# Performance work log

Hardware: AMD Instinct MI355X
Metric: run time of the kernel (lower is better)

Reference implementation:

```python
import jax, jax.numpy as jnp
import numpy as np

VOCAB, EMBED, HIDDEN, LAYERS = 256, 32, 32, 10
B, T = 1024, 1024


def setup_inputs() -> dict:
    key = jax.random.key(0)
    ks = jax.random.split(key, 8)
    s_e = 1.0  # nn.Embedding default init is N(0,1); scale others like uniform fan-in
    k_rnn = 1.0 / np.sqrt(HIDDEN)
    k_fc = 1.0 / np.sqrt(HIDDEN)
    x = jax.random.randint(ks[0], (B, T), 0, VOCAB, dtype=jnp.int64) if jax.config.jax_enable_x64 else jax.random.randint(ks[0], (B, T), 0, VOCAB, dtype=jnp.int32)
    emb = jax.random.normal(ks[1], (VOCAB, EMBED), dtype=jnp.float32) * s_e
    W_ih = jax.random.uniform(ks[2], (LAYERS, HIDDEN, EMBED), jnp.float32, -k_rnn, k_rnn)
    W_hh = jax.random.uniform(ks[3], (LAYERS, HIDDEN, HIDDEN), jnp.float32, -k_rnn, k_rnn)
    b_ih = jax.random.uniform(ks[4], (LAYERS, HIDDEN), jnp.float32, -k_rnn, k_rnn)
    b_hh = jax.random.uniform(ks[5], (LAYERS, HIDDEN), jnp.float32, -k_rnn, k_rnn)
    W_fc = jax.random.uniform(ks[6], (VOCAB, HIDDEN), jnp.float32, -k_fc, k_fc)
    b_fc = jax.random.uniform(ks[7], (VOCAB,), jnp.float32, -k_fc, k_fc)
    return {"x": x, "emb": emb, "W_ih": W_ih, "W_hh": W_hh,
            "b_ih": b_ih, "b_hh": b_hh, "W_fc": W_fc, "b_fc": b_fc}


def reference(x, emb, W_ih, W_hh, b_ih, b_hh, W_fc, b_fc):
    # Embedding lookup: [B, T, E]
    xe = emb[x]
    L = W_ih.shape[0]
    Bn = x.shape[0]
    h0 = jnp.zeros((L, Bn, W_hh.shape[-1]), dtype=xe.dtype)

    def step(h, xt):
        # h: [L, B, H]; xt: [B, E]
        inp = xt
        new_h = []
        for l in range(L):  # sequential across layers (true dependency)
            hl = jnp.tanh(inp @ W_ih[l].T + b_ih[l] + h[l] @ W_hh[l].T + b_hh[l])
            new_h.append(hl)
            inp = hl
        return jnp.stack(new_h), None

    hT, _ = jax.lax.scan(step, h0, jnp.swapaxes(xe, 0, 1))  # scan over T
    # out[:, -1, :] of top RNN layer == final hidden of last layer
    return hT[-1] @ W_fc.T + b_fc
```

## Files before the change

kernel.cpp:

```cpp
#include <hip/hip_runtime.h>

#define VOCABSZ 256
#define EMBED   32
#define HIDDEN  32
#define LAYERS  10
#define BATCH   1024
#define SEQ     1024
#define BPB     16
#define U       4
#define NITER   (SEQ / U + LAYERS - 1)

typedef _Float16 f16x8 __attribute__((ext_vector_type(8)));
typedef float    f32x4 __attribute__((ext_vector_type(4)));
typedef _Float16 h2    __attribute__((ext_vector_type(2)));

__device__ __forceinline__ unsigned pk(float a, float b) {
    h2 t; t[0] = (_Float16)a; t[1] = (_Float16)b;
    return __builtin_bit_cast(unsigned, t);
}
__device__ __forceinline__ f16x8 u2f(uint4 u) { return __builtin_bit_cast(f16x8, u); }

__device__ __forceinline__ float th(float c, float b2) {
    const float t = __builtin_fmaf(c, 2.8853900817779268f, b2);
#if __has_builtin(__builtin_amdgcn_exp2f)
    const float e = __builtin_amdgcn_exp2f(t);
#else
    const float e = __expf(0.6931471805599453f * t);
#endif
    const float r = __builtin_amdgcn_rcpf(1.0f + e);
    return __builtin_fmaf(-2.0f, r, 1.0f);
}

__device__ __forceinline__ uint4 mk_nat(const float* row, int g) {
    const float4 a = *(const float4*)(row + 8 * g);
    const float4 b = *(const float4*)(row + 8 * g + 4);
    return uint4{pk(a.x, a.y), pk(a.z, a.w), pk(b.x, b.y), pk(b.z, b.w)};
}
__device__ __forceinline__ uint4 mk_kp(const float* row, int g) {
    const float4 a = *(const float4*)(row + 4 * g);
    const float4 b = *(const float4*)(row + 16 + 4 * g);
    return uint4{pk(a.x, a.y), pk(a.z, a.w), pk(b.x, b.y), pk(b.z, b.w)};
}

__global__ __launch_bounds__(640, 1) void rnn_mfma(
    const int* __restrict__ x, const float* __restrict__ emb,
    const float* __restrict__ W_ih, const float* __restrict__ W_hh,
    const float* __restrict__ b_ih, const float* __restrict__ b_hh,
    float* __restrict__ h_out)
{
    __shared__ __align__(16) unsigned char hb[2 * LAYERS * U * 1024];

    const int tid   = threadIdx.x;
    const int w     = tid >> 6;
    const int lane  = tid & 63;
    const int bc    = lane & 15;
    const int g     = lane >> 4;
    const int bbase = blockIdx.x * BPB;

    for (int i = tid; i < (int)sizeof(hb) / 4; i += 640)
        ((unsigned*)hb)[i] = 0u;

    const float* ri0 = W_ih + (w * HIDDEN + bc)      * EMBED;
    const float* ri1 = W_ih + (w * HIDDEN + 16 + bc) * EMBED;
    const float* rh0 = W_hh + (w * HIDDEN + bc)      * HIDDEN;
    const float* rh1 = W_hh + (w * HIDDEN + 16 + bc) * HIDDEN;
    const uint4 wf00 = (w == 0) ? mk_nat(ri0, g) : mk_kp(ri0, g);
    const uint4 wf10 = (w == 0) ? mk_nat(ri1, g) : mk_kp(ri1, g);
    const uint4 wf01 = mk_kp(rh0, g);
    const uint4 wf11 = mk_kp(rh1, g);

    float bias2[8];
    #pragma unroll
    for (int m = 0; m < 2; ++m)
        #pragma unroll
        for (int r = 0; r < 4; ++r) {
            const int hid = w * HIDDEN + m * 16 + g * 4 + r;
            bias2[m * 4 + r] = 2.8853900817779268f * (b_ih[hid] + b_hh[hid]);
        }

    #define SL(p, l, u) ((((p) * LAYERS + (l)) * U + (u)) * 1024)
    const int off = g * 256 + bc * 16;

    uint4  cur[U];
    float4 eraw[U][2];
    int4   tok_pf;
    if (w == 0) {
        const int4 t4 = *(const int4*)(x + (bbase + bc) * SEQ);
        const int tk[U] = {t4.x, t4.y, t4.z, t4.w};
        #pragma unroll
        for (int u = 0; u < U; ++u) {
            const float4* ep = (const float4*)(emb + tk[u] * EMBED + g * 8);
            const float4 e0 = ep[0], e1 = ep[1];
            cur[u] = uint4{pk(e0.x, e0.y), pk(e0.z, e0.w), pk(e1.x, e1.y), pk(e1.z, e1.w)};
        }
        tok_pf = *(const int4*)(x + (bbase + bc) * SEQ + U);
    }

    uint4 bown = uint4{0, 0, 0, 0};

    auto body = [&](int it, int P) {
        __syncthreads();
        const int tb = (it - w) * U;
        if (tb < 0 || tb >= SEQ) return;

        const bool pf = (w == 0) && (tb + U < SEQ);
        if (pf) {
            const int tk[U] = {tok_pf.x, tok_pf.y, tok_pf.z, tok_pf.w};
            #pragma unroll
            for (int u = 0; u < U; ++u) {
                const float4* ep = (const float4*)(emb + tk[u] * EMBED + g * 8);
                eraw[u][0] = ep[0]; eraw[u][1] = ep[1];
            }
            if (tb + 2 * U < SEQ)
                tok_pf = *(const int4*)(x + (bbase + bc) * SEQ + tb + 2 * U);
        }

        uint4 bin[U];
        if (w == 0) {
            #pragma unroll
            for (int u = 0; u < U; ++u) bin[u] = cur[u];
        } else {
            #pragma unroll
            for (int u = 0; u < U; ++u)
                bin[u] = *(const uint4*)(hb + SL(P ^ 1, w - 1, u) + off);
        }
        f32x4 cin0[U], cin1[U];
        const f32x4 z = {0.f, 0.f, 0.f, 0.f};
        #pragma unroll
        for (int u = 0; u < U; ++u) {
            cin0[u] = __builtin_amdgcn_mfma_f32_16x16x32_f16(u2f(wf00), u2f(bin[u]), z, 0, 0, 0);
            cin1[u] = __builtin_amdgcn_mfma_f32_16x16x32_f16(u2f(wf10), u2f(bin[u]), z, 0, 0, 0);
        }

        #pragma unroll
        for (int u = 0; u < U; ++u) {
            const f32x4 c0 = __builtin_amdgcn_mfma_f32_16x16x32_f16(u2f(wf01), u2f(bown), cin0[u], 0, 0, 0);
            const f32x4 c1 = __builtin_amdgcn_mfma_f32_16x16x32_f16(u2f(wf11), u2f(bown), cin1[u], 0, 0, 0);

            float hv[8];
            #pragma unroll
            for (int r = 0; r < 4; ++r) {
                hv[r]     = th(c0[r], bias2[r]);
                hv[4 + r] = th(c1[r], bias2[4 + r]);
            }
            bown = uint4{pk(hv[0], hv[1]), pk(hv[2], hv[3]),
                         pk(hv[4], hv[5]), pk(hv[6], hv[7])};

            if (w < LAYERS - 1)
                *(uint4*)(hb + SL(P, w, u) + off) = bown;

            if (w == LAYERS - 1 && tb + u == SEQ - 1) {
                #pragma unroll
                for (int r = 0; r < 4; ++r) {
                    h_out[(bbase + bc) * HIDDEN + g * 4 + r]      = hv[r];
                    h_out[(bbase + bc) * HIDDEN + 16 + g * 4 + r] = hv[4 + r];
                }
            }
        }

        if (pf) {
            #pragma unroll
            for (int u = 0; u < U; ++u) {
                const float4 e0 = eraw[u][0], e1 = eraw[u][1];
                cur[u] = uint4{pk(e0.x, e0.y), pk(e0.z, e0.w), pk(e1.x, e1.y), pk(e1.z, e1.w)};
            }
        }
    };

    for (int it = 0; it < NITER + 1; it += 2) {
        body(it, 0);
        body(it + 1, 1);
    }
    #undef SL
}

__global__ __launch_bounds__(256) void rnn_fc(
    const float* __restrict__ h_fin, const float* __restrict__ W_fc,
    const float* __restrict__ b_fc, float* __restrict__ out)
{
    const int b = blockIdx.x;
    const int v = threadIdx.x;
    const float4* hr = (const float4*)(h_fin + b * HIDDEN);
    const float4* wr = (const float4*)(W_fc + v * HIDDEN);
    float acc = b_fc[v];
    #pragma unroll
    for (int c = 0; c < 8; ++c) {
        const float4 hv = hr[c], wv = wr[c];
        acc += hv.x * wv.x + hv.y * wv.y + hv.z * wv.z + hv.w * wv.w;
    }
    out[b * VOCABSZ + v] = acc;
}

extern "C" void kernel_launch(void* const* d_in, const int* in_sizes, int n_in,
                              void* d_out, int out_size, void* d_ws, size_t ws_size,
                              hipStream_t stream) {
    const int*   x    = (const int*)d_in[0];
    const float* emb  = (const float*)d_in[1];
    const float* W_ih = (const float*)d_in[2];
    const float* W_hh = (const float*)d_in[3];
    const float* b_ih = (const float*)d_in[4];
    const float* b_hh = (const float*)d_in[5];
    const float* W_fc = (const float*)d_in[6];
    const float* b_fc = (const float*)d_in[7];
    float* out   = (float*)d_out;
    float* h_fin = (float*)d_ws;

    rnn_mfma<<<BATCH / BPB, 640, 0, stream>>>(x, emb, W_ih, W_hh, b_ih, b_hh, h_fin);
    rnn_fc<<<BATCH, VOCABSZ, 0, stream>>>(h_fin, W_fc, b_fc, out);
}
```

Baseline: 535.0 us.

## Fuse final FC projection into RNN kernel via MFMA and double per-step unroll

Removes the separate FC kernel: the last layer's final hidden state is staged in shared memory and each wavefront computes 16-vocab tiles of the output projection with MFMA, then adds the bias. The timestep unroll U goes from 4 to 8, which halves the number of wavefront-pipeline stages and __syncthreads barriers but doubles the per-stage register and LDS buffers. The shared buffer drops the unused last-layer slot to offset part of that LDS growth. Risks are more register pressure and a longer pipeline fill and drain per stage.

```diff
diff --git a/kernel.cpp b/kernel.cpp
--- a/kernel.cpp
+++ b/kernel.cpp
@@ -7,8 +7,8 @@
 #define BATCH   1024
 #define SEQ     1024
 #define BPB     16
-#define U       4
-#define NITER   (SEQ / U + LAYERS - 1)
+#define U       8
+#define NBODY   (SEQ / U + LAYERS)
 
 typedef _Float16 f16x8 __attribute__((ext_vector_type(8)));
 typedef float    f32x4 __attribute__((ext_vector_type(4)));
@@ -42,13 +42,15 @@
     return uint4{pk(a.x, a.y), pk(a.z, a.w), pk(b.x, b.y), pk(b.z, b.w)};
 }
 
-__global__ __launch_bounds__(640, 1) void rnn_mfma(
+__global__ __launch_bounds__(640, 1) void rnn_fused(
     const int* __restrict__ x, const float* __restrict__ emb,
     const float* __restrict__ W_ih, const float* __restrict__ W_hh,
     const float* __restrict__ b_ih, const float* __restrict__ b_hh,
-    float* __restrict__ h_out)
+    const float* __restrict__ W_fc, const float* __restrict__ b_fc,
+    float* __restrict__ out)
 {
-    __shared__ __align__(16) unsigned char hb[2 * LAYERS * U * 1024];
+    __shared__ __align__(16) unsigned char hb[2 * (LAYERS - 1) * U * 1024];
+    __shared__ __align__(16) unsigned char fcs[1024];
 
     const int tid   = threadIdx.x;
     const int w     = tid >> 6;
@@ -78,25 +80,29 @@
             bias2[m * 4 + r] = 2.8853900817779268f * (b_ih[hid] + b_hh[hid]);
         }
 
-    #define SL(p, l, u) ((((p) * LAYERS + (l)) * U + (u)) * 1024)
+    #define SL(p, l, u_) ((((p) * (LAYERS - 1) + (l)) * U + (u_)) * 1024)
     const int off = g * 256 + bc * 16;
 
     uint4  cur[U];
     float4 eraw[U][2];
-    int4   tok_pf;
+    int    tokpf[U];
+    const int* xp = x + (bbase + bc) * SEQ;
     if (w == 0) {
-        const int4 t4 = *(const int4*)(x + (bbase + bc) * SEQ);
-        const int tk[U] = {t4.x, t4.y, t4.z, t4.w};
+        const int4 a = *(const int4*)(xp), b = *(const int4*)(xp + 4);
+        const int tk[U] = {a.x, a.y, a.z, a.w, b.x, b.y, b.z, b.w};
         #pragma unroll
         for (int u = 0; u < U; ++u) {
             const float4* ep = (const float4*)(emb + tk[u] * EMBED + g * 8);
             const float4 e0 = ep[0], e1 = ep[1];
             cur[u] = uint4{pk(e0.x, e0.y), pk(e0.z, e0.w), pk(e1.x, e1.y), pk(e1.z, e1.w)};
         }
-        tok_pf = *(const int4*)(x + (bbase + bc) * SEQ + U);
+        const int4 c = *(const int4*)(xp + 8), d = *(const int4*)(xp + 12);
+        tokpf[0] = c.x; tokpf[1] = c.y; tokpf[2] = c.z; tokpf[3] = c.w;
+        tokpf[4] = d.x; tokpf[5] = d.y; tokpf[6] = d.z; tokpf[7] = d.w;
     }
 
     uint4 bown = uint4{0, 0, 0, 0};
+    const f32x4 z = {0.f, 0.f, 0.f, 0.f};
 
     auto body = [&](int it, int P) {
         __syncthreads();
@@ -105,14 +111,17 @@
 
         const bool pf = (w == 0) && (tb + U < SEQ);
         if (pf) {
-            const int tk[U] = {tok_pf.x, tok_pf.y, tok_pf.z, tok_pf.w};
             #pragma unroll
             for (int u = 0; u < U; ++u) {
-                const float4* ep = (const float4*)(emb + tk[u] * EMBED + g * 8);
+                const float4* ep = (const float4*)(emb + tokpf[u] * EMBED + g * 8);
                 eraw[u][0] = ep[0]; eraw[u][1] = ep[1];
             }
-            if (tb + 2 * U < SEQ)
-                tok_pf = *(const int4*)(x + (bbase + bc) * SEQ + tb + 2 * U);
+            if (tb + 2 * U < SEQ) {
+                const int4 c = *(const int4*)(xp + tb + 2 * U);
+                const int4 d = *(const int4*)(xp + tb + 2 * U + 4);
+                tokpf[0] = c.x; tokpf[1] = c.y; tokpf[2] = c.z; tokpf[3] = c.w;
+                tokpf[4] = d.x; tokpf[5] = d.y; tokpf[6] = d.z; tokpf[7] = d.w;
+            }
         }
 
         uint4 bin[U];
@@ -125,7 +134,6 @@
                 bin[u] = *(const uint4*)(hb + SL(P ^ 1, w - 1, u) + off);
         }
         f32x4 cin0[U], cin1[U];
-        const f32x4 z = {0.f, 0.f, 0.f, 0.f};
         #pragma unroll
         for (int u = 0; u < U; ++u) {
             cin0[u] = __builtin_amdgcn_mfma_f32_16x16x32_f16(u2f(wf00), u2f(bin[u]), z, 0, 0, 0);
@@ -148,14 +156,6 @@
 
             if (w < LAYERS - 1)
                 *(uint4*)(hb + SL(P, w, u) + off) = bown;
-
-            if (w == LAYERS - 1 && tb + u == SEQ - 1) {
-                #pragma unroll
-                for (int r = 0; r < 4; ++r) {
-                    h_out[(bbase + bc) * HIDDEN + g * 4 + r]      = hv[r];
-                    h_out[(bbase + bc) * HIDDEN + 16 + g * 4 + r] = hv[4 + r];
-                }
-            }
         }
 
         if (pf) {
@@ -167,28 +167,26 @@
         }
     };
 
-    for (int it = 0; it < NITER + 1; it += 2) {
+    for (int it = 0; it < NBODY; it += 2) {
         body(it, 0);
         body(it + 1, 1);
     }
     #undef SL
-}
-
-__global__ __launch_bounds__(256) void rnn_fc(
-    const float* __restrict__ h_fin, const float* __restrict__ W_fc,
-    const float* __restrict__ b_fc, float* __restrict__ out)
-{
-    const int b = blockIdx.x;
-    const int v = threadIdx.x;
-    const float4* hr = (const float4*)(h_fin + b * HIDDEN);
-    const float4* wr = (const float4*)(W_fc + v * HIDDEN);
-    float acc = b_fc[v];
+
+    if (w == LAYERS - 1) *(uint4*)(fcs + off) = bown;
+    __syncthreads();
+    const uint4 bfc = *(const uint4*)(fcs + off);
     #pragma unroll
-    for (int c = 0; c < 8; ++c) {
-        const float4 hv = hr[c], wv = wr[c];
-        acc += hv.x * wv.x + hv.y * wv.y + hv.z * wv.z + hv.w * wv.w;
+    for (int rep = 0; rep < 2; ++rep) {
+        const int vt = w + rep * LAYERS;
+        if (vt < VOCABSZ / 16) {
+            const uint4 afc = mk_kp(W_fc + (vt * 16 + bc) * HIDDEN, g);
+            const f32x4 c = __builtin_amdgcn_mfma_f32_16x16x32_f16(u2f(afc), u2f(bfc), z, 0, 0, 0);
+            const float4 b4 = *(const float4*)(b_fc + vt * 16 + 4 * g);
+            const float4 o  = {c[0] + b4.x, c[1] + b4.y, c[2] + b4.z, c[3] + b4.w};
+            *(float4*)(out + (bbase + bc) * VOCABSZ + vt * 16 + 4 * g) = o;
+        }
     }
-    out[b * VOCABSZ + v] = acc;
 }
 
 extern "C" void kernel_launch(void* const* d_in, const int* in_sizes, int n_in,
@@ -202,9 +200,8 @@
     const float* b_hh = (const float*)d_in[5];
     const float* W_fc = (const float*)d_in[6];
     const float* b_fc = (const float*)d_in[7];
-    float* out   = (float*)d_out;
-    float* h_fin = (float*)d_ws;
-
-    rnn_mfma<<<BATCH / BPB, 640, 0, stream>>>(x, emb, W_ih, W_hh, b_ih, b_hh, h_fin);
-    rnn_fc<<<BATCH, VOCABSZ, 0, stream>>>(h_fin, W_fc, b_fc, out);
-}
+    float* out = (float*)d_out;
+
+    rnn_fused<<<BATCH / BPB, 640, 0, stream>>>(x, emb, W_ih, W_hh, b_ih, b_hh,
+                                               W_fc, b_fc, out);
+}
```

Result: slower. 677.9 us (+26.7%).
